# Optimization experiments

Measured on AMD Instinct MI355X. Metric: run time of the kernel, lower is better.

The kernel has to match this reference:

```python
import jax, jax.numpy as jnp
import numpy as np

B, S, D, E, N = 2, 1024, 1024, 64, 16  # batch, seq, model_dim, embedding_dim, num_splats


def setup_inputs() -> dict:
    key = jax.random.key(0)
    ks = jax.random.split(key, 8)
    inv_sqrt_d = 1.0 / np.sqrt(D)
    return {
        "token_embeddings": jax.random.normal(ks[0], (B, S, D), jnp.float32),
        # position encoder Linear(D, E)
        "pos_W": jax.random.normal(ks[1], (D, E), jnp.float32) * inv_sqrt_d,
        "pos_b": jnp.zeros((E,), jnp.float32),
        "positional_bias": jax.random.normal(ks[2], (1024, E), jnp.float32) * 0.01,
        "splat_positions": jax.random.normal(ks[3], (N, E), jnp.float32) * 0.2,
        "splat_log_scales": jnp.zeros((N,), jnp.float32),
        # q/k/v Linear(D, D, bias=False)
        "q_W": jax.random.normal(ks[4], (D, D), jnp.float32) * inv_sqrt_d,
        "k_W": jax.random.normal(ks[5], (D, D), jnp.float32) * inv_sqrt_d,
        "v_W": jax.random.normal(ks[6], (D, D), jnp.float32) * inv_sqrt_d,
        "splat_gates": jnp.full((N,), 0.5, jnp.float32),
        "residual_weight": jnp.asarray(0.8, jnp.float32),
        "ln_w": jnp.ones((D,), jnp.float32),
        "ln_b": jnp.zeros((D,), jnp.float32),
    }


def reference(token_embeddings, pos_W, pos_b, positional_bias, splat_positions,
              splat_log_scales, q_W, k_W, v_W, splat_gates, residual_weight,
              ln_w, ln_b):
    b, s, d = token_embeddings.shape
    # token positions in splat embedding space: tanh(Linear(x)) + pos_bias[:S]
    positions = jnp.tanh(token_embeddings @ pos_W + pos_b) + positional_bias[:s][None]  # [B,S,E]
    # spatial influence per splat: Gaussian of distance, clamped scales, floor 0.01
    diff = positions[:, :, None, :] - splat_positions[None, None]  # [B,S,N,E]
    dist_sq = jnp.sum(diff * diff, axis=-1)                         # [B,S,N]
    scales = jnp.clip(jnp.exp(splat_log_scales), 0.3, 2.0)
    influence = jnp.maximum(jnp.exp(-0.5 * dist_sq / (scales * scales)), 0.01)  # [B,S,N]

    q = token_embeddings @ q_W
    k = token_embeddings @ k_W
    v = token_embeddings @ v_W

    w = jnp.transpose(influence, (2, 0, 1))      # [N,B,S]
    qw = q[None] * w[..., None]                  # [N,B,S,D]
    kw = k[None] * w[..., None]
    scores = jnp.einsum('nbid,nbjd->nbij', qw, kw) / jnp.sqrt(jnp.asarray(d, jnp.float32))
    causal = jnp.tril(jnp.ones((s, s), bool))
    scores = jnp.where(causal[None, None], scores, -1e9)
    attn = jax.nn.softmax(scores, axis=-1)       # [N,B,S,S]
    out = jnp.einsum('nbij,bjd->nbid', attn, v)  # [N,B,S,D]

    gates = jax.nn.sigmoid(splat_gates)[:, None, None, None]
    combined = jnp.mean(out * gates, axis=0)     # [B,S,D]

    rw = jax.nn.sigmoid(residual_weight)
    o = rw * token_embeddings + (1.0 - rw) * combined
    # LayerNorm (eps=1e-5)
    mu = jnp.mean(o, axis=-1, keepdims=True)
    var = jnp.mean((o - mu) ** 2, axis=-1, keepdims=True)
    return (o - mu) / jnp.sqrt(var + 1e-5) * ln_w + ln_b
```

## Files before the change

kernel.cpp:

```cpp
#include <hip/hip_runtime.h>
#include <hip/hip_bf16.h>
#include <hip/hip_fp16.h>

using bf16 = __hip_bfloat16;
typedef __attribute__((ext_vector_type(8))) short short8;
typedef __attribute__((ext_vector_type(4))) float f32x4;

static constexpr int Bb = 2, Ss = 1024, Dd = 1024, Ee = 64, Nn = 16;

struct Params {
    const float *X, *posW, *posB, *pbias, *spos, *lsc, *qW, *kW, *vW, *gates, *rwp, *lnw, *lnb;
    bf16 *Xb, *Wt, *WpT, *QKV, *Vt, *Aav;
    __half *wh;
    float *qk[4], *cb[4], *out;
};

__device__ __forceinline__ unsigned short f2bfr(float f) {
    __hip_bfloat16 h = __float2bfloat16(f);
    return *reinterpret_cast<unsigned short*>(&h);
}

#define GL_LDS(gp, lp) __builtin_amdgcn_global_load_lds( \
    (const __attribute__((address_space(1))) void*)(gp), \
    (__attribute__((address_space(3))) void*)(lp), 16, 0, 0)

__device__ __forceinline__ void do_transpose_f2b(
    const float* __restrict__ in, bf16* __restrict__ out,
    int R, int C, int bx, int by, char* sm)
{
    float (*tile)[65] = (float(*)[65])sm;
    int tx = threadIdx.x & 63, ty = threadIdx.x >> 6;
    int r0 = by * 64, c0 = bx * 64;
    #pragma unroll
    for (int i = 0; i < 16; ++i)
        tile[ty + i*4][tx] = in[(long)(r0 + ty + i*4)*C + c0 + tx];
    __syncthreads();
    #pragma unroll
    for (int i = 0; i < 16; ++i)
        out[(long)(c0 + ty + i*4)*R + r0 + tx] = __float2bfloat16(tile[tx][ty + i*4]);
    __syncthreads();
}

__device__ __forceinline__ void do_gemm64(
    const bf16* __restrict__ Ab, const bf16* __restrict__ Bw, float* __restrict__ C,
    int Nc, int m0, int n0, int kBeg, int kEnd, float scale, char* sm)
{
    short* lA = (short*)sm;
    short* lB = (short*)(sm + 8192);
    int tid = threadIdx.x, wid = tid >> 6, lane = tid & 63;
    int wn = wid * 32, r16 = lane & 15, quad = lane >> 4;

    f32x4 acc[4][2];
    #pragma unroll
    for (int i = 0; i < 4; ++i)
        #pragma unroll
        for (int j = 0; j < 2; ++j)
            #pragma unroll
            for (int c = 0; c < 4; ++c) acc[i][j][c] = 0.f;

    const short* Ag = (const short*)Ab;
    const short* Bg = (const short*)Bw;

    int arow[2], akg[2], brow[4], bkg[4];
    #pragma unroll
    for (int j = 0; j < 2; ++j) {
        int c = tid + j*256; arow[j] = c >> 3; akg[j] = (c & 7) ^ (arow[j] & 7);
    }
    #pragma unroll
    for (int j = 0; j < 4; ++j) {
        int c = tid + j*256; brow[j] = c >> 3; bkg[j] = (c & 7) ^ (brow[j] & 7);
    }

    for (int k0 = kBeg; k0 < kEnd; k0 += 64) {
        __syncthreads();
        #pragma unroll
        for (int j = 0; j < 2; ++j)
            GL_LDS(Ag + (long)(m0 + arow[j])*1024 + k0 + akg[j]*8, lA + (tid + j*256)*8);
        #pragma unroll
        for (int j = 0; j < 4; ++j)
            GL_LDS(Bg + (long)(n0 + brow[j])*1024 + k0 + bkg[j]*8, lB + (tid + j*256)*8);
        __syncthreads();

        #pragma unroll
        for (int kk = 0; kk < 2; ++kk) {
            int kc = kk*4 + quad;
            short8 af[4], bfv[2];
            #pragma unroll
            for (int i = 0; i < 4; ++i) {
                int r = i*16 + r16;
                af[i] = *(const short8*)(lA + r*64 + (kc ^ (r & 7))*8);
            }
            #pragma unroll
            for (int j = 0; j < 2; ++j) {
                int r = wn + j*16 + r16;
                bfv[j] = *(const short8*)(lB + r*64 + (kc ^ (r & 7))*8);
            }
            #pragma unroll
            for (int i = 0; i < 4; ++i)
                #pragma unroll
                for (int j = 0; j < 2; ++j)
                    acc[i][j] = __builtin_amdgcn_mfma_f32_16x16x32_bf16(af[i], bfv[j], acc[i][j], 0, 0, 0);
        }
    }

    #pragma unroll
    for (int i = 0; i < 4; ++i)
        #pragma unroll
        for (int j = 0; j < 2; ++j)
            #pragma unroll
            for (int rr = 0; rr < 4; ++rr)
                C[(long)(m0 + i*16 + quad*4 + rr)*Nc + n0 + wn + j*16 + r16] =
                    acc[i][j][rr] * scale;
}

template<int OUT_MODE>
__device__ __forceinline__ void do_gemm128(
    const bf16* __restrict__ Ab, const bf16* __restrict__ Bw, void* __restrict__ Cv,
    int Nc, int m0, int n0, char* sm)
{
    short* lA = (short*)sm;
    short* lB = (short*)(sm + 16384);
    int tid = threadIdx.x, wid = tid >> 6, lane = tid & 63;
    int wm = (wid >> 1) * 64, wnn = (wid & 1) * 64;
    int r16 = lane & 15, quad = lane >> 4;

    f32x4 acc[4][4];
    #pragma unroll
    for (int i = 0; i < 4; ++i)
        #pragma unroll
        for (int j = 0; j < 4; ++j)
            #pragma unroll
            for (int c = 0; c < 4; ++c) acc[i][j][c] = 0.f;

    const short* Ag = (const short*)Ab;
    const short* Bg = (const short*)Bw;

    int rowc[4], kgc[4];
    #pragma unroll
    for (int j = 0; j < 4; ++j) {
        int c = tid + j*256; rowc[j] = c >> 3; kgc[j] = (c & 7) ^ (rowc[j] & 7);
    }

    for (int k0 = 0; k0 < 1024; k0 += 64) {
        __syncthreads();
        #pragma unroll
        for (int j = 0; j < 4; ++j)
            GL_LDS(Ag + (long)(m0 + rowc[j])*1024 + k0 + kgc[j]*8, lA + (tid + j*256)*8);
        #pragma unroll
        for (int j = 0; j < 4; ++j)
            GL_LDS(Bg + (long)(n0 + rowc[j])*1024 + k0 + kgc[j]*8, lB + (tid + j*256)*8);
        __syncthreads();

        #pragma unroll
        for (int kk = 0; kk < 2; ++kk) {
            int kc = kk*4 + quad;
            short8 af[4], bfv[4];
            #pragma unroll
            for (int i = 0; i < 4; ++i) {
                int r = wm + i*16 + r16;
                af[i] = *(const short8*)(lA + r*64 + (kc ^ (r & 7))*8);
            }
            #pragma unroll
            for (int j = 0; j < 4; ++j) {
                int r = wnn + j*16 + r16;
                bfv[j] = *(const short8*)(lB + r*64 + (kc ^ (r & 7))*8);
            }
            #pragma unroll
            for (int i = 0; i < 4; ++i)
                #pragma unroll
                for (int j = 0; j < 4; ++j)
                    acc[i][j] = __builtin_amdgcn_mfma_f32_16x16x32_bf16(af[i], bfv[j], acc[i][j], 0, 0, 0);
        }
    }

    if (OUT_MODE == 1) {
        bf16* C = (bf16*)Cv;
        #pragma unroll
        for (int i = 0; i < 4; ++i)
            #pragma unroll
            for (int j = 0; j < 4; ++j)
                #pragma unroll
                for (int rr = 0; rr < 4; ++rr)
                    C[(long)(m0 + wm + i*16 + quad*4 + rr)*Nc + n0 + wnn + j*16 + r16] =
                        __float2bfloat16(acc[i][j][rr]);
    } else {
        __syncthreads();
        bf16 (*lt)[132] = (bf16(*)[132])sm;
        #pragma unroll
        for (int i = 0; i < 4; ++i)
            #pragma unroll
            for (int j = 0; j < 4; ++j)
                #pragma unroll
                for (int rr = 0; rr < 4; ++rr)
                    lt[wnn + j*16 + r16][wm + i*16 + quad*4 + rr] =
                        __float2bfloat16(acc[i][j][rr]);
        __syncthreads();
        bf16* Vb = (bf16*)Cv + (long)(m0 >> 10) * Dd * Ss;
        int s0 = m0 & (Ss - 1);
        int colBase = wid * 32 + (lane >> 4);
        int idx = (lane & 15) * 8;
        #pragma unroll
        for (int it = 0; it < 8; ++it) {
            int col = colBase + it * 4;
            ushort4 v0 = *(const ushort4*)&lt[col][idx];
            ushort4 v1 = *(const ushort4*)&lt[col][idx + 4];
            *(ushort4*)(Vb + (long)(n0 + col)*Ss + s0 + idx)     = v0;
            *(ushort4*)(Vb + (long)(n0 + col)*Ss + s0 + idx + 4) = v1;
        }
    }
}

__device__ __forceinline__ void do_pos(const Params& p, int m0, char* sm)
{
    short* lA = (short*)sm;
    short* lB = (short*)(sm + 4096);
    float (*P)[65]  = (float(*)[65])(sm + 8192);
    float (*sp)[65] = (float(*)[65])(sm + 8192 + 64*65*4);

    int tid = threadIdx.x, wid = tid >> 6, lane = tid & 63;
    int r16 = lane & 15, quad = lane >> 4;

    for (int idx = tid; idx < 16*64; idx += 256)
        sp[idx >> 6][idx & 63] = p.spos[idx];

    f32x4 acc[4];
    #pragma unroll
    for (int j = 0; j < 4; ++j)
        #pragma unroll
        for (int c = 0; c < 4; ++c) acc[j][c] = 0.f;

    int ra = tid >> 2, ka = (tid & 3) * 8;
    const short* Ag = (const short*)p.Xb;
    const short* Bg = (const short*)p.WpT;

    for (int k0 = 0; k0 < Dd; k0 += 32) {
        __syncthreads();
        GL_LDS(Ag + (long)(m0+ra)*1024 + k0 + ka, lA + tid*8);
        GL_LDS(Bg + (long)ra*1024 + k0 + ka,      lB + tid*8);
        __syncthreads();

        short8 af = *(const short8*)(lA + (wid*16 + r16)*32 + quad*8);
        #pragma unroll
        for (int j = 0; j < 4; ++j) {
            short8 bfv = *(const short8*)(lB + (j*16 + r16)*32 + quad*8);
            acc[j] = __builtin_amdgcn_mfma_f32_16x16x32_bf16(af, bfv, acc[j], 0, 0, 0);
        }
    }

    #pragma unroll
    for (int j = 0; j < 4; ++j)
        #pragma unroll
        for (int rr = 0; rr < 4; ++rr) {
            int rl  = wid*16 + quad*4 + rr;
            int col = j*16 + r16;
            int srow = (m0 + rl) & (Ss - 1);
            P[rl][col] = tanhf(acc[j][rr] + p.posB[col]) + p.pbias[srow*Ee + col];
        }
    __syncthreads();

    int n  = tid & 15;
    int rb = (tid >> 4) * 4;
    float sc = __expf(p.lsc[n]);
    sc = fminf(fmaxf(sc, 0.3f), 2.0f);
    float inv2 = -0.5f / (sc * sc);
    #pragma unroll
    for (int rr = 0; rr < 4; ++rr) {
        int row = rb + rr;
        float d2 = 0.f;
        #pragma unroll 16
        for (int e = 0; e < 64; ++e) {
            float df = P[row][e] - sp[n][e];
            d2 += df * df;
        }
        float infl = fmaxf(__expf(d2 * inv2), 0.01f);
        p.wh[(long)(m0 + row)*Nn + n] = __float2half(infl);
    }
}

__global__ __launch_bounds__(256) void k_prep(Params p)
{
    __shared__ __align__(16) char sm[64*65*4];
    int z = blockIdx.z;
    if (z < 3) {
        const float* w = (z == 0) ? p.qW : (z == 1) ? p.kW : p.vW;
        do_transpose_f2b(w, p.Wt + (long)z*Dd*Dd, Dd, Dd, blockIdx.x, blockIdx.y, sm);
    } else if (blockIdx.x == 0) {
        do_transpose_f2b(p.posW, p.WpT, Dd, Ee, 0, blockIdx.y, sm);
    } else {
        int job = blockIdx.y * 15 + (blockIdx.x - 1);
        const float4* src = (const float4*)p.X;
        ushort4* dst = (ushort4*)p.Xb;
        for (int idx = job*256 + (int)threadIdx.x; idx < Bb*Ss*Dd/4; idx += 240*256) {
            float4 v = src[idx];
            ushort4 y;
            y.x = f2bfr(v.x); y.y = f2bfr(v.y); y.z = f2bfr(v.z); y.w = f2bfr(v.w);
            dst[idx] = y;
        }
    }
}

__global__ __launch_bounds__(256) void k_qkv_pos(Params p)
{
    __shared__ __align__(16) char sm[33792];
    int job = blockIdx.x;
    if (job < 384) {
        int z = job >> 7, t = job & 127;
        int bm = t >> 3, bn = t & 7;
        if (z < 2)
            do_gemm128<1>(p.Xb, p.Wt + (long)z*Dd*Dd, p.QKV + (long)z*2048*1024,
                          Dd, bm*128, bn*128, sm);
        else
            do_gemm128<2>(p.Xb, p.Wt + (long)2*Dd*Dd, p.Vt,
                          Dd, bm*128, bn*128, sm);
    } else {
        do_pos(p, (job - 384)*64, sm);
    }
}

__global__ __launch_bounds__(256) void k_qkt(Params p)
{
    __shared__ __align__(16) char sm[24576];
    int job = blockIdx.x;
    int h = job & 3, pairIdx = job >> 2;
    int b = pairIdx / 72, t = pairIdx % 72;
    int acc = 0, bm = 0, bn = 0;
    #pragma unroll
    for (int u = 0; u < 16; ++u) {
        int c = (u >> 1) + 1;
        if (t < acc + c) { bm = u; bn = t - acc; break; }
        acc += c;
    }
    const bf16* Qb = p.QKV + (long)b*Ss*Dd;
    const bf16* Kb = p.QKV + (long)2048*1024 + (long)b*Ss*Dd;
    float* dst = p.qk[h] + (long)b*Ss*Ss;
    do_gemm64(Qb, Kb, dst, Ss, bm*64, bn*128, h*256, h*256 + 256, 0.03125f, sm);
}

__global__ __launch_bounds__(256) void k_softmax(Params p)
{
    __shared__ __align__(16) char sm[36864 + 256];
    __half2 (*wt)[9] = (__half2(*)[9])sm;
    float (*wi4)[16] = (float(*)[16])(sm + 36864);

    int base = blockIdx.x * 4, b = blockIdx.y;
    int tid = threadIdx.x, wid = tid >> 6, lane = tid & 63;
    int imax = base + 3;

    const __half*  whb  = p.wh + (long)b*Ss*Nn;
    const __half2* whb2 = (const __half2*)whb;

    for (int j = tid; j <= imax; j += 256) {
        #pragma unroll
        for (int h = 0; h < 8; ++h)
            wt[j][h] = whb2[j*8 + h];
    }
    if (tid < 64) wi4[tid >> 4][tid & 15] =
        __half2float(whb[(long)(base + (tid >> 4))*16 + (tid & 15)]);
    __syncthreads();

    int i = base + wid;
    long roff = ((long)b*Ss + i)*Ss;
    const float* q0 = p.qk[0] + roff;
    const float* q1 = p.qk[1] + roff;
    const float* q2 = p.qk[2] + roff;
    const float* q3 = p.qk[3] + roff;
    bf16* arow      = p.Aav + roff;

    float wiR[16], l[16];
    #pragma unroll
    for (int n = 0; n < 16; ++n) { wiR[n] = wi4[wid][n]; l[n] = 0.f; }

    for (int j = lane; j <= i; j += 64) {
        float q = (q0[j] + q1[j]) + (q2[j] + q3[j]);
        #pragma unroll
        for (int h = 0; h < 8; ++h) {
            float2 f = __half22float2(wt[j][h]);
            l[2*h]     += __expf(wiR[2*h]     * f.x * q);
            l[2*h + 1] += __expf(wiR[2*h + 1] * f.y * q);
        }
    }
    #pragma unroll
    for (int n = 0; n < 16; ++n)
        #pragma unroll
        for (int off = 32; off > 0; off >>= 1)
            l[n] += __shfl_xor(l[n], off);

    float coef[16];
    #pragma unroll
    for (int n = 0; n < 16; ++n) {
        float g  = p.gates[n];
        float sg = 1.f / (1.f + __expf(-g));
        coef[n]  = sg / (16.f * l[n]);
    }

    for (int j = lane; j < Ss; j += 64) {
        float a = 0.f;
        if (j <= i) {
            float q = (q0[j] + q1[j]) + (q2[j] + q3[j]);
            #pragma unroll
            for (int h = 0; h < 8; ++h) {
                float2 f = __half22float2(wt[j][h]);
                a += coef[2*h]     * __expf(wiR[2*h]     * f.x * q);
                a += coef[2*h + 1] * __expf(wiR[2*h + 1] * f.y * q);
            }
        }
        arow[j] = __float2bfloat16(a);
    }
}

__global__ __launch_bounds__(256) void k_av(Params p)
{
    __shared__ __align__(16) char sm[24576];
    int job = blockIdx.x;
    int b  = job / 320;
    int r  = job % 320;
    int bn = r / 40;
    int u  = r % 40;
    int acc = 0, bm = 0, h = 0;
    #pragma unroll
    for (int m = 0; m < 16; ++m) {
        int c = (m >> 2) + 1;
        if (u < acc + c) { bm = m; h = u - acc; break; }
        acc += c;
    }
    int kBeg = h * 256;
    int kEnd = (bm + 1) * 64; if (kEnd > kBeg + 256) kEnd = kBeg + 256;

    const bf16* Ab = p.Aav + (long)b*Ss*Ss;
    const bf16* Bw = p.Vt + (long)b*Dd*Ss;
    float* dst = p.cb[h] + (long)b*Ss*Dd;
    do_gemm64(Ab, Bw, dst, Dd, bm*64, bn*128, kBeg, kEnd, 1.f, sm);
}

__global__ __launch_bounds__(256) void k_epilogue(Params p)
{
    __shared__ float rs[4], rq[4];
    long row = blockIdx.x;
    int tid = threadIdx.x, wid = tid >> 6, lane = tid & 63;
    float rw = 1.f / (1.f + __expf(-p.rwp[0]));

    int s = (int)(row & (Ss - 1));
    float4 c = ((const float4*)(p.cb[0] + row*Dd))[tid];
    #pragma unroll
    for (int h = 1; h < 4; ++h) {
        if (s >= h*256) {
            float4 ch = ((const float4*)(p.cb[h] + row*Dd))[tid];
            c.x += ch.x; c.y += ch.y; c.z += ch.z; c.w += ch.w;
        }
    }
    float4 xv = ((const float4*)(p.X + row*Dd))[tid];

    float o[4];
    o[0] = rw * xv.x + (1.f - rw) * c.x;
    o[1] = rw * xv.y + (1.f - rw) * c.y;
    o[2] = rw * xv.z + (1.f - rw) * c.z;
    o[3] = rw * xv.w + (1.f - rw) * c.w;

    float sm1 = o[0] + o[1] + o[2] + o[3];
    float sq  = o[0]*o[0] + o[1]*o[1] + o[2]*o[2] + o[3]*o[3];
    #pragma unroll
    for (int off = 32; off > 0; off >>= 1) { sm1 += __shfl_xor(sm1, off); sq += __shfl_xor(sq, off); }
    if (lane == 0) { rs[wid] = sm1; rq[wid] = sq; }
    __syncthreads();
    sm1 = rs[0] + rs[1] + rs[2] + rs[3];
    sq  = rq[0] + rq[1] + rq[2] + rq[3];
    float mu  = sm1 * (1.f/1024.f);
    float var = sq * (1.f/1024.f) - mu*mu;
    float inv = rsqrtf(var + 1e-5f);

    float4 lw = ((const float4*)p.lnw)[tid];
    float4 lb = ((const float4*)p.lnb)[tid];
    float4 y;
    y.x = (o[0] - mu)*inv*lw.x + lb.x;
    y.y = (o[1] - mu)*inv*lw.y + lb.y;
    y.z = (o[2] - mu)*inv*lw.z + lb.z;
    y.w = (o[3] - mu)*inv*lw.w + lb.w;
    ((float4*)(p.out + row*Dd))[tid] = y;
}

extern "C" void kernel_launch(void* const* d_in, const int* in_sizes, int n_in,
                              void* d_out, int out_size, void* d_ws, size_t ws_size,
                              hipStream_t stream)
{
    Params prm;
    prm.X     = (const float*)d_in[0];
    prm.posW  = (const float*)d_in[1];
    prm.posB  = (const float*)d_in[2];
    prm.pbias = (const float*)d_in[3];
    prm.spos  = (const float*)d_in[4];
    prm.lsc   = (const float*)d_in[5];
    prm.qW    = (const float*)d_in[6];
    prm.kW    = (const float*)d_in[7];
    prm.vW    = (const float*)d_in[8];
    prm.gates = (const float*)d_in[9];
    prm.rwp   = (const float*)d_in[10];
    prm.lnw   = (const float*)d_in[11];
    prm.lnb   = (const float*)d_in[12];

    char* ws = (char*)d_ws;
    size_t off = 0;
    prm.Xb  = (bf16*)(ws + off);   off += (size_t)Bb*Ss*Dd*2;
    prm.Wt  = (bf16*)(ws + off);   off += (size_t)3*Dd*Dd*2;
    prm.WpT = (bf16*)(ws + off);   off += (size_t)Ee*Dd*2;
    prm.QKV = (bf16*)(ws + off);   off += (size_t)2*2048*1024*2;
    prm.Vt  = (bf16*)(ws + off);   off += (size_t)Bb*Dd*Ss*2;
    prm.Aav = (bf16*)(ws + off);   off += (size_t)Bb*Ss*Ss*2;
    prm.wh  = (__half*)(ws + off); off += (size_t)Bb*Ss*Nn*2;
    for (int h = 0; h < 4; ++h) { prm.qk[h] = (float*)(ws + off); off += (size_t)Bb*Ss*Ss*4; }
    for (int h = 0; h < 4; ++h) { prm.cb[h] = (float*)(ws + off); off += (size_t)Bb*Ss*Dd*4; }
    prm.out = (float*)d_out;
    (void)ws_size;

    k_prep    <<<dim3(16,16,4), 256, 0, stream>>>(prm);
    k_qkv_pos <<<416,            256, 0, stream>>>(prm);
    k_qkt     <<<576,            256, 0, stream>>>(prm);
    k_softmax <<<dim3(256, 2),   256, 0, stream>>>(prm);
    k_av      <<<640,            256, 0, stream>>>(prm);
    k_epilogue<<<2048,           256, 0, stream>>>(prm);
}
```

Baseline: 164.1 us.

## Double-buffer LDS in GEMMs and cache summed scores in softmax

After: 160.2 us, median of 2. -2.4%, faster.

```diff
diff --git a/kernel.cpp b/kernel.cpp
--- a/kernel.cpp
+++ b/kernel.cpp
@@ -45,8 +45,6 @@
     const bf16* __restrict__ Ab, const bf16* __restrict__ Bw, float* __restrict__ C,
     int Nc, int m0, int n0, int kBeg, int kEnd, float scale, char* sm)
 {
-    short* lA = (short*)sm;
-    short* lB = (short*)(sm + 8192);
     int tid = threadIdx.x, wid = tid >> 6, lane = tid & 63;
     int wn = wid * 32, r16 = lane & 15, quad = lane >> 4;
 
@@ -71,16 +69,24 @@
         int c = tid + j*256; brow[j] = c >> 3; bkg[j] = (c & 7) ^ (brow[j] & 7);
     }
 
+    auto stage = [&](int k0, int cr) {
+        short* sA = (short*)(sm + cr*24576);
+        short* sB = (short*)(sm + cr*24576 + 8192);
+        #pragma unroll
+        for (int j = 0; j < 2; ++j)
+            GL_LDS(Ag + (long)(m0 + arow[j])*1024 + k0 + akg[j]*8, sA + (tid + j*256)*8);
+        #pragma unroll
+        for (int j = 0; j < 4; ++j)
+            GL_LDS(Bg + (long)(n0 + brow[j])*1024 + k0 + bkg[j]*8, sB + (tid + j*256)*8);
+    };
+
+    stage(kBeg, 0);
+    __syncthreads();
+    int cur = 0;
     for (int k0 = kBeg; k0 < kEnd; k0 += 64) {
-        __syncthreads();
-        #pragma unroll
-        for (int j = 0; j < 2; ++j)
-            GL_LDS(Ag + (long)(m0 + arow[j])*1024 + k0 + akg[j]*8, lA + (tid + j*256)*8);
-        #pragma unroll
-        for (int j = 0; j < 4; ++j)
-            GL_LDS(Bg + (long)(n0 + brow[j])*1024 + k0 + bkg[j]*8, lB + (tid + j*256)*8);
-        __syncthreads();
-
+        if (k0 + 64 < kEnd) stage(k0 + 64, cur ^ 1);
+        short* lA = (short*)(sm + cur*24576);
+        short* lB = (short*)(sm + cur*24576 + 8192);
         #pragma unroll
         for (int kk = 0; kk < 2; ++kk) {
             int kc = kk*4 + quad;
@@ -101,6 +107,8 @@
                 for (int j = 0; j < 2; ++j)
                     acc[i][j] = __builtin_amdgcn_mfma_f32_16x16x32_bf16(af[i], bfv[j], acc[i][j], 0, 0, 0);
         }
+        __syncthreads();
+        cur ^= 1;
     }
 
     #pragma unroll
@@ -118,8 +126,6 @@
     const bf16* __restrict__ Ab, const bf16* __restrict__ Bw, void* __restrict__ Cv,
     int Nc, int m0, int n0, char* sm)
 {
-    short* lA = (short*)sm;
-    short* lB = (short*)(sm + 16384);
     int tid = threadIdx.x, wid = tid >> 6, lane = tid & 63;
     int wm = (wid >> 1) * 64, wnn = (wid & 1) * 64;
     int r16 = lane & 15, quad = lane >> 4;
@@ -141,16 +147,24 @@
         int c = tid + j*256; rowc[j] = c >> 3; kgc[j] = (c & 7) ^ (rowc[j] & 7);
     }
 
+    auto stage = [&](int k0, int cr) {
+        short* sA = (short*)(sm + cr*32768);
+        short* sB = (short*)(sm + cr*32768 + 16384);
+        #pragma unroll
+        for (int j = 0; j < 4; ++j)
+            GL_LDS(Ag + (long)(m0 + rowc[j])*1024 + k0 + kgc[j]*8, sA + (tid + j*256)*8);
+        #pragma unroll
+        for (int j = 0; j < 4; ++j)
+            GL_LDS(Bg + (long)(n0 + rowc[j])*1024 + k0 + kgc[j]*8, sB + (tid + j*256)*8);
+    };
+
+    stage(0, 0);
+    __syncthreads();
+    int cur = 0;
     for (int k0 = 0; k0 < 1024; k0 += 64) {
-        __syncthreads();
-        #pragma unroll
-        for (int j = 0; j < 4; ++j)
-            GL_LDS(Ag + (long)(m0 + rowc[j])*1024 + k0 + kgc[j]*8, lA + (tid + j*256)*8);
-        #pragma unroll
-        for (int j = 0; j < 4; ++j)
-            GL_LDS(Bg + (long)(n0 + rowc[j])*1024 + k0 + kgc[j]*8, lB + (tid + j*256)*8);
-        __syncthreads();
-
+        if (k0 + 64 < 1024) stage(k0 + 64, cur ^ 1);
+        short* lA = (short*)(sm + cur*32768);
+        short* lB = (short*)(sm + cur*32768 + 16384);
         #pragma unroll
         for (int kk = 0; kk < 2; ++kk) {
             int kc = kk*4 + quad;
@@ -171,6 +185,8 @@
                 for (int j = 0; j < 4; ++j)
                     acc[i][j] = __builtin_amdgcn_mfma_f32_16x16x32_bf16(af[i], bfv[j], acc[i][j], 0, 0, 0);
         }
+        __syncthreads();
+        cur ^= 1;
     }
 
     if (OUT_MODE == 1) {
@@ -212,10 +228,8 @@
 
 __device__ __forceinline__ void do_pos(const Params& p, int m0, char* sm)
 {
-    short* lA = (short*)sm;
-    short* lB = (short*)(sm + 4096);
-    float (*P)[65]  = (float(*)[65])(sm + 8192);
-    float (*sp)[65] = (float(*)[65])(sm + 8192 + 64*65*4);
+    float (*P)[65]  = (float(*)[65])(sm + 16384);
+    float (*sp)[65] = (float(*)[65])(sm + 16384 + 64*65*4);
 
     int tid = threadIdx.x, wid = tid >> 6, lane = tid & 63;
     int r16 = lane & 15, quad = lane >> 4;
@@ -233,18 +247,28 @@
     const short* Ag = (const short*)p.Xb;
     const short* Bg = (const short*)p.WpT;
 
+    auto stage = [&](int k0, int cr) {
+        short* sA = (short*)(sm + cr*8192);
+        short* sB = (short*)(sm + cr*8192 + 4096);
+        GL_LDS(Ag + (long)(m0+ra)*1024 + k0 + ka, sA + tid*8);
+        GL_LDS(Bg + (long)ra*1024 + k0 + ka,      sB + tid*8);
+    };
+
+    stage(0, 0);
+    __syncthreads();
+    int cur = 0;
     for (int k0 = 0; k0 < Dd; k0 += 32) {
-        __syncthreads();
-        GL_LDS(Ag + (long)(m0+ra)*1024 + k0 + ka, lA + tid*8);
-        GL_LDS(Bg + (long)ra*1024 + k0 + ka,      lB + tid*8);
-        __syncthreads();
-
+        if (k0 + 32 < Dd) stage(k0 + 32, cur ^ 1);
+        short* lA = (short*)(sm + cur*8192);
+        short* lB = (short*)(sm + cur*8192 + 4096);
         short8 af = *(const short8*)(lA + (wid*16 + r16)*32 + quad*8);
         #pragma unroll
         for (int j = 0; j < 4; ++j) {
             short8 bfv = *(const short8*)(lB + (j*16 + r16)*32 + quad*8);
             acc[j] = __builtin_amdgcn_mfma_f32_16x16x32_bf16(af, bfv, acc[j], 0, 0, 0);
         }
+        __syncthreads();
+        cur ^= 1;
     }
 
     #pragma unroll
@@ -301,7 +325,7 @@
 
 __global__ __launch_bounds__(256) void k_qkv_pos(Params p)
 {
-    __shared__ __align__(16) char sm[33792];
+    __shared__ __align__(16) char sm[65536];
     int job = blockIdx.x;
     if (job < 384) {
         int z = job >> 7, t = job & 127;
@@ -319,7 +343,7 @@
 
 __global__ __launch_bounds__(256) void k_qkt(Params p)
 {
-    __shared__ __align__(16) char sm[24576];
+    __shared__ __align__(16) char sm[49152];
     int job = blockIdx.x;
     int h = job & 3, pairIdx = job >> 2;
     int b = pairIdx / 72, t = pairIdx % 72;
@@ -338,9 +362,10 @@
 
 __global__ __launch_bounds__(256) void k_softmax(Params p)
 {
-    __shared__ __align__(16) char sm[36864 + 256];
+    __shared__ __align__(16) char sm[36864 + 256 + 16384];
     __half2 (*wt)[9] = (__half2(*)[9])sm;
     float (*wi4)[16] = (float(*)[16])(sm + 36864);
+    float (*qc)[Ss]  = (float(*)[Ss])(sm + 36864 + 256);
 
     int base = blockIdx.x * 4, b = blockIdx.y;
     int tid = threadIdx.x, wid = tid >> 6, lane = tid & 63;
@@ -372,6 +397,7 @@
 
     for (int j = lane; j <= i; j += 64) {
         float q = (q0[j] + q1[j]) + (q2[j] + q3[j]);
+        qc[wid][j] = q;
         #pragma unroll
         for (int h = 0; h < 8; ++h) {
             float2 f = __half22float2(wt[j][h]);
@@ -393,10 +419,11 @@
         coef[n]  = sg / (16.f * l[n]);
     }
 
-    for (int j = lane; j < Ss; j += 64) {
+    int jLim = (i | 63) + 1;
+    for (int j = lane; j < jLim; j += 64) {
         float a = 0.f;
         if (j <= i) {
-            float q = (q0[j] + q1[j]) + (q2[j] + q3[j]);
+            float q = qc[wid][j];
             #pragma unroll
             for (int h = 0; h < 8; ++h) {
                 float2 f = __half22float2(wt[j][h]);
@@ -410,7 +437,7 @@
 
 __global__ __launch_bounds__(256) void k_av(Params p)
 {
-    __shared__ __align__(16) char sm[24576];
+    __shared__ __align__(16) char sm[49152];
     int job = blockIdx.x;
     int b  = job / 320;
     int r  = job % 320;
```
